# Performance work log

Measured on AMD Instinct MI355X. Metric: run time of the kernel, lower is better.

## Reference

```python
import jax, jax.numpy as jnp
import numpy as np

B, N, C, F, E, K = 4, 4096, 1024, 4096, 8, 2

def setup_inputs() -> dict:
    key = jax.random.key(0)
    ks = jax.random.split(key, 6)
    x = jax.random.normal(ks[0], (B, N, C), dtype=jnp.float32)
    router_w = jax.random.normal(ks[1], (E, C), dtype=jnp.float32) * 0.02  # nn.Linear weight [out,in]
    w1 = jax.random.normal(ks[2], (E, C, F), dtype=jnp.float32) * (1.0 / np.sqrt(C))
    b1 = jnp.zeros((E, F), dtype=jnp.float32)
    w2 = jax.random.normal(ks[3], (E, F, C), dtype=jnp.float32) * (1.0 / np.sqrt(F))
    b2 = jnp.zeros((E, C), dtype=jnp.float32)
    return {"x": x, "router_w": router_w, "w1": w1, "b1": b1, "w2": w2, "b2": b2}

def reference(x, router_w, w1, b1, w2, b2):
    Bx, Nx, Cx = x.shape
    xf = x.reshape(-1, Cx)                                  # [T, C]
    logits = xf @ router_w.T                                # [T, E]
    probs = jax.nn.softmax(logits, axis=-1)
    top_w, top_i = jax.lax.top_k(probs, K)                  # [T, K]
    top_w = top_w / (jnp.sum(top_w, axis=-1, keepdims=True) + 1e-9)
    out = jnp.zeros_like(xf)
    for e in range(E):
        # combine weight for expert e per token (0 if not routed)
        gate = jnp.sum(jnp.where(top_i == e, top_w, 0.0), axis=-1)   # [T]
        h = jax.nn.gelu(xf @ w1[e] + b1[e], approximate=False)       # [T, F]
        y = h @ w2[e] + b2[e]                                        # [T, C]
        out = out + gate[:, None] * y
    return out.reshape(Bx, Nx, Cx)
```

## Files before the change

### kernel.cpp

```cpp
#include <hip/hip_runtime.h>
#include <hip/hip_fp16.h>

#define T_TOK 16384
#define C_DIM 1024
#define F_DIM 4096
#define E_NUM 8

typedef _Float16 half8 __attribute__((ext_vector_type(8)));
typedef _Float16 half4v __attribute__((ext_vector_type(4)));
typedef float f32x4 __attribute__((ext_vector_type(4)));

static constexpr size_t META_OFF  = 0;
static constexpr size_t XB_OFF    = 256;
static constexpr size_t W1T_OFF   = XB_OFF  + (size_t)2*T_TOK*C_DIM;
static constexpr size_t W2T_OFF   = W1T_OFF + (size_t)2*E_NUM*C_DIM*F_DIM;
static constexpr size_t HB_OFF    = W2T_OFF + (size_t)2*E_NUM*C_DIM*F_DIM;
static constexpr size_t YB_OFF    = HB_OFF  + (size_t)2*T_TOK*2*F_DIM;
static constexpr size_t TOK_OFF   = YB_OFF  + (size_t)2*T_TOK*2*C_DIM;
static constexpr size_t GATE_OFF  = TOK_OFF + (size_t)4*E_NUM*T_TOK;
static constexpr size_t TSLOT_OFF = GATE_OFF+ (size_t)4*E_NUM*T_TOK;
static constexpr size_t EPAIR_OFF = TSLOT_OFF + (size_t)4*T_TOK*2;
static constexpr size_t GPAIR_OFF = EPAIR_OFF + (size_t)4*T_TOK;
static constexpr size_t WS_NEED   = GPAIR_OFF + (size_t)8*T_TOK;

__device__ __forceinline__ void async16(void* lds, const void* g) {
  __builtin_amdgcn_global_load_lds((const __attribute__((address_space(1))) unsigned int*)g,
                                   (__attribute__((address_space(3))) unsigned int*)lds,
                                   16, 0, 0);
}

__device__ __forceinline__ void stagger(int bid) {
  int s = (bid >> 8) & 3;
  for (int i = 0; i < s * 5; ++i) __builtin_amdgcn_s_sleep(2);
}

__global__ __launch_bounds__(256) void transpose_cast_kernel(const float* __restrict__ in,
                                                             _Float16* __restrict__ outp,
                                                             int R, int Cc) {
  __shared__ float tile[64][65];
  int e = blockIdx.z;
  const float* ip = in + (size_t)e * R * Cc;
  _Float16* op = outp + (size_t)e * R * Cc;
  int c0 = blockIdx.x * 64, r0 = blockIdx.y * 64;
  int tid = threadIdx.x;
  int lr = tid >> 4, lc = (tid & 15) * 4;
  #pragma unroll
  for (int d = 0; d < 4; ++d) {
    int row = lr + d * 16;
    float4 v = *(const float4*)(ip + (size_t)(r0 + row) * Cc + c0 + lc);
    tile[row][lc]     = v.x;
    tile[row][lc + 1] = v.y;
    tile[row][lc + 2] = v.z;
    tile[row][lc + 3] = v.w;
  }
  __syncthreads();
  int oc = tid >> 3, or8 = (tid & 7) * 8;
  #pragma unroll
  for (int d = 0; d < 2; ++d) {
    int c = oc + d * 32;
    half8 h;
    #pragma unroll
    for (int j = 0; j < 8; ++j) h[j] = (_Float16)tile[or8 + j][c];
    *(half8*)(op + (size_t)(c0 + c) * R + r0 + or8) = h;
  }
}

__global__ __launch_bounds__(256) void router_kernel(const float* __restrict__ x,
                                                     const float* __restrict__ rw,
                                                     int* __restrict__ epair,
                                                     float2* __restrict__ gpair,
                                                     _Float16* __restrict__ xb) {
  int wv = threadIdx.x >> 6, l = threadIdx.x & 63;
  int t = blockIdx.x * 4 + wv;
  const float* xr = x + (size_t)t * C_DIM;
  double acc[E_NUM] = {};
  #pragma unroll
  for (int j = 0; j < 4; ++j) {
    float4 xv = *(const float4*)(xr + j * 256 + l * 4);
    half4v hv;
    hv[0] = (_Float16)xv.x; hv[1] = (_Float16)xv.y;
    hv[2] = (_Float16)xv.z; hv[3] = (_Float16)xv.w;
    *(half4v*)(xb + (size_t)t * C_DIM + j * 256 + l * 4) = hv;
    #pragma unroll
    for (int e = 0; e < E_NUM; ++e) {
      float4 w4 = *(const float4*)(rw + (size_t)e * C_DIM + j * 256 + l * 4);
      acc[e] += (double)xv.x * w4.x + (double)xv.y * w4.y +
                (double)xv.z * w4.z + (double)xv.w * w4.w;
    }
  }
  #pragma unroll
  for (int e = 0; e < E_NUM; ++e)
    #pragma unroll
    for (int off = 32; off; off >>= 1)
      acc[e] += __shfl_xor(acc[e], off, 64);

  if (l == 0) {
    double m = acc[0];
    #pragma unroll
    for (int e = 1; e < E_NUM; ++e) m = acc[e] > m ? acc[e] : m;
    double p[E_NUM], s = 0.0;
    #pragma unroll
    for (int e = 0; e < E_NUM; ++e) { p[e] = exp(acc[e] - m); s += p[e]; }
    int i0 = 0; double b0 = p[0];
    #pragma unroll
    for (int e = 1; e < E_NUM; ++e) if (p[e] > b0) { b0 = p[e]; i0 = e; }
    int i1 = -1; double b1v = -1.0;
    #pragma unroll
    for (int e = 0; e < E_NUM; ++e) if (e != i0 && p[e] > b1v) { b1v = p[e]; i1 = e; }
    double q0 = b0 / s, q1 = b1v / s;
    double den = q0 + q1 + 1e-9;
    epair[t] = i0 | (i1 << 8);
    gpair[t] = make_float2((float)(q0 / den), (float)(q1 / den));
  }
}

__global__ __launch_bounds__(1024) void assign_kernel(const int* __restrict__ epair,
                                                      const float2* __restrict__ gpair,
                                                      int* __restrict__ counts,
                                                      int* __restrict__ tok,
                                                      float* __restrict__ gate,
                                                      int* __restrict__ tslot) {
  __shared__ int wsum[16];
  __shared__ int wbase[16];
  __shared__ int stot;
  int myE = blockIdx.x;
  int tid = threadIdx.x, wid = tid >> 6, lane = tid & 63;
  int base = 0;
  for (int it = 0; it < (T_TOK * 2) / 1024; ++it) {
    int idx = it * 1024 + tid;
    int t = idx >> 1, k = idx & 1;
    int ep = epair[t];
    int e = (k ? (ep >> 8) : ep) & 0xff;
    bool f = (e == myE);
    unsigned long long mask = __ballot(f);
    int lanep = __popcll(mask & ((1ull << lane) - 1ull));
    if (lane == 0) wsum[wid] = __popcll(mask);
    __syncthreads();
    if (tid == 0) {
      int s = 0;
      #pragma unroll
      for (int i = 0; i < 16; ++i) { wbase[i] = s; s += wsum[i]; }
      stot = s;
    }
    __syncthreads();
    if (f) {
      int slot = base + wbase[wid] + lanep;
      float2 g = gpair[t];
      tok[myE * T_TOK + slot] = t;
      gate[myE * T_TOK + slot] = k ? g.y : g.x;
      tslot[idx] = (myE << 24) | slot;
    }
    base += stot;
  }
  if (tid == 0) counts[myE] = base;
}

__global__ void plan_kernel(int* meta) {
  if (threadIdx.x == 0 && blockIdx.x == 0) {
    int ro = 0, t128 = 0;
    meta[8] = 0; meta[17] = 0;
    for (int e = 0; e < E_NUM; ++e) {
      int c = meta[e];
      ro += c; t128 += (c + 127) >> 7;
      meta[9 + e] = ro; meta[18 + e] = t128;
    }
  }
}


__global__ __launch_bounds__(512) void gemm1_kernel(const _Float16* __restrict__ xb,
                                                    const _Float16* __restrict__ w1t,
                                                    const float* __restrict__ b1,
                                                    _Float16* __restrict__ hbuf,
                                                    const int* __restrict__ tok,
                                                    const int* __restrict__ meta) {
  __shared__ _Float16 smem[24576];
  __shared__ int tokLds[128];

  int bid = blockIdx.x;
  int swz = (bid & 7) * 528 + (bid >> 3);
  int band = swz >> 7, rem = swz & 127;
  int nt = rem >> 3;
  int mt = band * 8 + (rem & 7);
  if (mt >= meta[17 + E_NUM]) return;
  stagger(bid);
  int e = 0;
  while (mt >= meta[18 + e]) ++e;
  int ne = meta[e];
  int r0 = (mt - meta[17 + e]) << 7;
  int valid = ne - r0; if (valid > 128) valid = 128;

  int tid = threadIdx.x;
  if (tid < 128) {
    int r = tid < valid ? tid : valid - 1;
    tokLds[tid] = tok[e * T_TOK + r0 + r];
  }
  __syncthreads();

  int srow = tid >> 3, c8 = tid & 7;
  int ch = c8 ^ (srow & 7);
  const _Float16* aLo = xb + (size_t)tokLds[srow] * C_DIM + ch * 8;
  const _Float16* aHi = xb + (size_t)tokLds[srow + 64] * C_DIM + ch * 8;
  const _Float16* bS  = w1t + ((size_t)e * F_DIM + nt * 256 + srow) * C_DIM + ch * 8;

  char* SM = (char*)smem;
  char* dst = SM + (size_t)tid * 16;

  int w = tid >> 6, l = tid & 63;
  int wm = w >> 2, wn = w & 3;
  int rl = l & 15, q = l >> 4;
  int sw0 = (q ^ (rl & 7)) * 16;
  int sw1 = ((4 + q) ^ (rl & 7)) * 16;
  int aBy = wm * 8192 + rl * 128;
  int bBy = 16384 + wn * 8192 + rl * 128;

  f32x4 acc[4][4] = {};
  constexpr int NT = C_DIM / 64;
  for (int kt = 0; kt < NT; ++kt) {
    __syncthreads();
    int ko = kt * 64;
    async16(dst,          aLo + ko);
    async16(dst + 8192,   aHi + ko);
    async16(dst + 16384,  bS + ko);
    async16(dst + 24576,  bS + (size_t) 64 * C_DIM + ko);
    async16(dst + 32768,  bS + (size_t)128 * C_DIM + ko);
    async16(dst + 40960,  bS + (size_t)192 * C_DIM + ko);
    __syncthreads();
    #pragma unroll
    for (int ks = 0; ks < 2; ++ks) {
      int sw = ks ? sw1 : sw0;
      half8 af[4], bf[4];
      #pragma unroll
      for (int m = 0; m < 4; ++m)
        af[m] = *(const half8*)(SM + aBy + m * 2048 + sw);
      #pragma unroll
      for (int n = 0; n < 4; ++n)
        bf[n] = *(const half8*)(SM + bBy + n * 2048 + sw);
      #pragma unroll
      for (int m = 0; m < 4; ++m)
        #pragma unroll
        for (int n = 0; n < 4; ++n)
          acc[m][n] = __builtin_amdgcn_mfma_f32_16x16x32_f16(af[m], bf[n], acc[m][n], 0, 0, 0);
    }
  }

  int hbase = meta[8 + e] + r0;
  float bv[4];
  #pragma unroll
  for (int n = 0; n < 4; ++n)
    bv[n] = b1[(size_t)e * F_DIM + nt * 256 + wn * 64 + n * 16 + rl];
  #pragma unroll
  for (int m = 0; m < 4; ++m) {
    int rb = wm * 64 + m * 16 + q * 4;
    #pragma unroll
    for (int n = 0; n < 4; ++n) {
      int col = nt * 256 + wn * 64 + n * 16 + rl;
      #pragma unroll
      for (int r = 0; r < 4; ++r) {
        int rr = rb + r;
        if (rr < valid) {
          float pre = acc[m][n][r] + bv[n];
          float g = 0.5f * pre * (1.0f + erff(pre * 0.70710678118654752f));
          hbuf[(size_t)(hbase + rr) * F_DIM + col] = (_Float16)g;
        }
      }
    }
  }
}

__global__ __launch_bounds__(512) void gemm2_kernel(const _Float16* __restrict__ hbuf,
                                                    const _Float16* __restrict__ w2t,
                                                    const float* __restrict__ b2,
                                                    _Float16* __restrict__ ybuf,
                                                    const float* __restrict__ gate,
                                                    const int* __restrict__ meta) {
  __shared__ _Float16 smem[24576];
  __shared__ float gateLds[128];

  int bid = blockIdx.x;
  int swz = (bid & 7) * 132 + (bid >> 3);
  int band = swz >> 5, rem = swz & 31;
  int nt = rem >> 3;
  int mt = band * 8 + (rem & 7);
  if (mt >= meta[17 + E_NUM]) return;
  stagger(bid);
  int e = 0;
  while (mt >= meta[18 + e]) ++e;
  int ne = meta[e];
  int r0 = (mt - meta[17 + e]) << 7;
  int valid = ne - r0; if (valid > 128) valid = 128;
  int hbase = meta[8 + e] + r0;

  int tid = threadIdx.x;
  if (tid < 128) {
    int r = tid < valid ? tid : valid - 1;
    gateLds[tid] = gate[e * T_TOK + r0 + r];
  }
  __syncthreads();

  int srow = tid >> 3, c8 = tid & 7;
  int ch = c8 ^ (srow & 7);
  int rcLo = srow      < valid ? srow      : valid - 1;
  int rcHi = srow + 64 < valid ? srow + 64 : valid - 1;
  const _Float16* aLo = hbuf + (size_t)(hbase + rcLo) * F_DIM + ch * 8;
  const _Float16* aHi = hbuf + (size_t)(hbase + rcHi) * F_DIM + ch * 8;
  const _Float16* bS  = w2t + ((size_t)e * C_DIM + nt * 256 + srow) * F_DIM + ch * 8;

  char* SM = (char*)smem;
  char* dst = SM + (size_t)tid * 16;

  int w = tid >> 6, l = tid & 63;
  int wm = w >> 2, wn = w & 3;
  int rl = l & 15, q = l >> 4;
  int sw0 = (q ^ (rl & 7)) * 16;
  int sw1 = ((4 + q) ^ (rl & 7)) * 16;
  int aBy = wm * 8192 + rl * 128;
  int bBy = 16384 + wn * 8192 + rl * 128;

  f32x4 acc[4][4] = {};
  constexpr int NT = F_DIM / 64;
  for (int kt = 0; kt < NT; ++kt) {
    __syncthreads();
    int ko = kt * 64;
    async16(dst,          aLo + ko);
    async16(dst + 8192,   aHi + ko);
    async16(dst + 16384,  bS + ko);
    async16(dst + 24576,  bS + (size_t) 64 * F_DIM + ko);
    async16(dst + 32768,  bS + (size_t)128 * F_DIM + ko);
    async16(dst + 40960,  bS + (size_t)192 * F_DIM + ko);
    __syncthreads();
    #pragma unroll
    for (int ks = 0; ks < 2; ++ks) {
      int sw = ks ? sw1 : sw0;
      half8 af[4], bf[4];
      #pragma unroll
      for (int m = 0; m < 4; ++m)
        af[m] = *(const half8*)(SM + aBy + m * 2048 + sw);
      #pragma unroll
      for (int n = 0; n < 4; ++n)
        bf[n] = *(const half8*)(SM + bBy + n * 2048 + sw);
      #pragma unroll
      for (int m = 0; m < 4; ++m)
        #pragma unroll
        for (int n = 0; n < 4; ++n)
          acc[m][n] = __builtin_amdgcn_mfma_f32_16x16x32_f16(af[m], bf[n], acc[m][n], 0, 0, 0);
    }
  }

  float bv[4];
  #pragma unroll
  for (int n = 0; n < 4; ++n)
    bv[n] = b2[(size_t)e * C_DIM + nt * 256 + wn * 64 + n * 16 + rl];
  #pragma unroll
  for (int m = 0; m < 4; ++m) {
    int rb = wm * 64 + m * 16 + q * 4;
    #pragma unroll
    for (int n = 0; n < 4; ++n) {
      int col = nt * 256 + wn * 64 + n * 16 + rl;
      #pragma unroll
      for (int r = 0; r < 4; ++r) {
        int rr = rb + r;
        if (rr < valid) {
          float val = gateLds[rr] * (acc[m][n][r] + bv[n]);
          ybuf[(size_t)(hbase + rr) * C_DIM + col] = (_Float16)val;
        }
      }
    }
  }
}

__global__ __launch_bounds__(256) void combine_kernel(const _Float16* __restrict__ ybuf,
                                                      const int* __restrict__ tslot,
                                                      const int* __restrict__ meta,
                                                      float* __restrict__ out) {
  int gid = blockIdx.x * 256 + threadIdx.x;
  int t = gid >> 7;
  int cc = (gid & 127) << 3;
  int s0 = tslot[t * 2], s1 = tslot[t * 2 + 1];
  size_t r0 = (size_t)meta[8 + (s0 >> 24)] + (s0 & 0xFFFFFF);
  size_t r1 = (size_t)meta[8 + (s1 >> 24)] + (s1 & 0xFFFFFF);
  half8 y0 = *(const half8*)(ybuf + r0 * C_DIM + cc);
  half8 y1 = *(const half8*)(ybuf + r1 * C_DIM + cc);
  float4 o0, o1;
  o0.x = (float)y0[0] + (float)y1[0];
  o0.y = (float)y0[1] + (float)y1[1];
  o0.z = (float)y0[2] + (float)y1[2];
  o0.w = (float)y0[3] + (float)y1[3];
  o1.x = (float)y0[4] + (float)y1[4];
  o1.y = (float)y0[5] + (float)y1[5];
  o1.z = (float)y0[6] + (float)y1[6];
  o1.w = (float)y0[7] + (float)y1[7];
  *(float4*)(out + (size_t)t * C_DIM + cc) = o0;
  *(float4*)(out + (size_t)t * C_DIM + cc + 4) = o1;
}

extern "C" void kernel_launch(void* const* d_in, const int* in_sizes, int n_in,
                              void* d_out, int out_size, void* d_ws, size_t ws_size,
                              hipStream_t stream) {
  (void)in_sizes; (void)n_in; (void)out_size;
  if (!d_ws || ws_size < WS_NEED) return;

  const float* x  = (const float*)d_in[0];
  const float* rw = (const float*)d_in[1];
  const float* w1 = (const float*)d_in[2];
  const float* b1 = (const float*)d_in[3];
  const float* w2 = (const float*)d_in[4];
  const float* b2 = (const float*)d_in[5];
  float* out = (float*)d_out;

  char* ws = (char*)d_ws;
  int*       meta  = (int*)(ws + META_OFF);
  _Float16*  xb    = (_Float16*)(ws + XB_OFF);
  _Float16*  w1t   = (_Float16*)(ws + W1T_OFF);
  _Float16*  w2t   = (_Float16*)(ws + W2T_OFF);
  _Float16*  hbuf  = (_Float16*)(ws + HB_OFF);
  _Float16*  ybuf  = (_Float16*)(ws + YB_OFF);
  int*       tok   = (int*)(ws + TOK_OFF);
  float*     gate  = (float*)(ws + GATE_OFF);
  int*       tslot = (int*)(ws + TSLOT_OFF);
  int*       epair = (int*)(ws + EPAIR_OFF);
  float2*    gpair = (float2*)(ws + GPAIR_OFF);

  hipMemsetAsync(meta, 0, 256, stream);

  transpose_cast_kernel<<<dim3(F_DIM / 64, C_DIM / 64, E_NUM), 256, 0, stream>>>(w1, w1t, C_DIM, F_DIM);
  transpose_cast_kernel<<<dim3(C_DIM / 64, F_DIM / 64, E_NUM), 256, 0, stream>>>(w2, w2t, F_DIM, C_DIM);
  router_kernel<<<T_TOK / 4, 256, 0, stream>>>(x, rw, epair, gpair, xb);
  assign_kernel<<<E_NUM, 1024, 0, stream>>>(epair, gpair, meta, tok, gate, tslot);
  plan_kernel<<<1, 64, 0, stream>>>(meta);

  gemm1_kernel<<<264 * 16, 512, 0, stream>>>(xb, w1t, b1, hbuf, tok, meta);
  gemm2_kernel<<<264 * 4, 512, 0, stream>>>(hbuf, w2t, b2, ybuf, gate, meta);
  combine_kernel<<<(T_TOK * (C_DIM / 8)) / 256, 256, 0, stream>>>(ybuf, tslot, meta, out);
}
```

Before: 934.4 us.

## Enlarge gemm1 to 256x256 tiles with double-buffered async LDS pipeline

The first expert GEMM moves from 128x256 tiles with a single LDS buffer and two barriers per k-step to 256x256 tiles. Two 64 KB LDS stages are filled by async loads that are interleaved with MFMA phases, using explicit vmcnt waits, s_barrier and s_setprio. The plan kernel now also computes per-expert prefix counts of 256-row tiles, and the grid and its swizzle constants are resized to match. The aim is to hide global-load latency and raise arithmetic intensity. In exchange it uses much more LDS and more accumulator registers (occupancy drops to one block per CU), pads experts to 256 rows, and drops the launch stagger.

```diff
diff --git a/kernel.cpp b/kernel.cpp
--- a/kernel.cpp
+++ b/kernel.cpp
@@ -157,16 +157,50 @@
 
 __global__ void plan_kernel(int* meta) {
   if (threadIdx.x == 0 && blockIdx.x == 0) {
-    int ro = 0, t128 = 0;
-    meta[8] = 0; meta[17] = 0;
+    int ro = 0, t128 = 0, t256 = 0;
+    meta[8] = 0; meta[17] = 0; meta[26] = 0;
     for (int e = 0; e < E_NUM; ++e) {
       int c = meta[e];
-      ro += c; t128 += (c + 127) >> 7;
-      meta[9 + e] = ro; meta[18 + e] = t128;
-    }
-  }
-}
-
+      ro += c; t128 += (c + 127) >> 7; t256 += (c + 255) >> 8;
+      meta[9 + e] = ro; meta[18 + e] = t128; meta[27 + e] = t256;
+    }
+  }
+}
+
+
+#define VM4 asm volatile("s_waitcnt vmcnt(4)" ::: "memory")
+#define VM6 asm volatile("s_waitcnt vmcnt(6)" ::: "memory")
+#define VM8 asm volatile("s_waitcnt vmcnt(8)" ::: "memory")
+
+#define STA(b,s,t) async16(SM + (b)*65536 + (s)*8192 + (size_t)tid*16, aSeg[s] + (t)*64)
+#define STB(b,s,t) async16(SM + (b)*65536 + 32768 + (s)*8192 + (size_t)tid*16, bSeg[s] + (t)*64)
+
+#define PH_LOAD(TB, MH, NH)                                                    \
+    _Pragma("unroll")                                                          \
+    for (int i2 = 0; i2 < 4; ++i2) {                                           \
+      af[i2*2]   = *(const half8*)(SM + (TB) + (MH)*16384 + aOff[i2] + sw0);   \
+      af[i2*2+1] = *(const half8*)(SM + (TB) + (MH)*16384 + aOff[i2] + sw1);   \
+    }                                                                          \
+    _Pragma("unroll")                                                          \
+    for (int j2 = 0; j2 < 2; ++j2) {                                           \
+      bf[j2*2]   = *(const half8*)(SM + (TB) + 32768 + (NH)*16384 + bOff[j2] + sw0); \
+      bf[j2*2+1] = *(const half8*)(SM + (TB) + 32768 + (NH)*16384 + bOff[j2] + sw1); \
+    }
+
+#define PH_MMA(MH, NH)                                                         \
+    __builtin_amdgcn_s_barrier();                                              \
+    __builtin_amdgcn_s_setprio(1);                                             \
+    _Pragma("unroll")                                                          \
+    for (int i2 = 0; i2 < 4; ++i2)                                             \
+      _Pragma("unroll")                                                        \
+      for (int j2 = 0; j2 < 2; ++j2) {                                         \
+        acc[(MH)*4+i2][(NH)*2+j2] = __builtin_amdgcn_mfma_f32_16x16x32_f16(    \
+            af[i2*2], bf[j2*2], acc[(MH)*4+i2][(NH)*2+j2], 0, 0, 0);           \
+        acc[(MH)*4+i2][(NH)*2+j2] = __builtin_amdgcn_mfma_f32_16x16x32_f16(    \
+            af[i2*2+1], bf[j2*2+1], acc[(MH)*4+i2][(NH)*2+j2], 0, 0, 0);       \
+      }                                                                        \
+    __builtin_amdgcn_s_setprio(0);                                             \
+    __builtin_amdgcn_s_barrier();
 
 __global__ __launch_bounds__(512) void gemm1_kernel(const _Float16* __restrict__ xb,
                                                     const _Float16* __restrict__ w1t,
@@ -174,24 +208,23 @@
                                                     _Float16* __restrict__ hbuf,
                                                     const int* __restrict__ tok,
                                                     const int* __restrict__ meta) {
-  __shared__ _Float16 smem[24576];
-  __shared__ int tokLds[128];
+  __shared__ _Float16 smem[65536];
+  __shared__ int tokLds[256];
 
   int bid = blockIdx.x;
-  int swz = (bid & 7) * 528 + (bid >> 3);
+  int swz = (bid & 7) * 272 + (bid >> 3);
   int band = swz >> 7, rem = swz & 127;
   int nt = rem >> 3;
   int mt = band * 8 + (rem & 7);
-  if (mt >= meta[17 + E_NUM]) return;
-  stagger(bid);
+  if (mt >= meta[26 + E_NUM]) return;
   int e = 0;
-  while (mt >= meta[18 + e]) ++e;
+  while (mt >= meta[27 + e]) ++e;
   int ne = meta[e];
-  int r0 = (mt - meta[17 + e]) << 7;
-  int valid = ne - r0; if (valid > 128) valid = 128;
+  int r0 = (mt - meta[26 + e]) << 8;
+  int valid = ne - r0; if (valid > 256) valid = 256;
 
   int tid = threadIdx.x;
-  if (tid < 128) {
+  if (tid < 256) {
     int r = tid < valid ? tid : valid - 1;
     tokLds[tid] = tok[e * T_TOK + r0 + r];
   }
@@ -199,69 +232,91 @@
 
   int srow = tid >> 3, c8 = tid & 7;
   int ch = c8 ^ (srow & 7);
-  const _Float16* aLo = xb + (size_t)tokLds[srow] * C_DIM + ch * 8;
-  const _Float16* aHi = xb + (size_t)tokLds[srow + 64] * C_DIM + ch * 8;
-  const _Float16* bS  = w1t + ((size_t)e * F_DIM + nt * 256 + srow) * C_DIM + ch * 8;
-
+  const _Float16* aSeg[4];
+  const _Float16* bSeg[4];
+  #pragma unroll
+  for (int s = 0; s < 4; ++s) {
+    aSeg[s] = xb + (size_t)tokLds[s * 64 + srow] * C_DIM + ch * 8;
+    bSeg[s] = w1t + ((size_t)e * F_DIM + nt * 256 + s * 64 + srow) * C_DIM + ch * 8;
+  }
   char* SM = (char*)smem;
-  char* dst = SM + (size_t)tid * 16;
 
   int w = tid >> 6, l = tid & 63;
-  int wm = w >> 2, wn = w & 3;
+  int wh = w >> 2, wn = w & 3;
   int rl = l & 15, q = l >> 4;
   int sw0 = (q ^ (rl & 7)) * 16;
   int sw1 = ((4 + q) ^ (rl & 7)) * 16;
-  int aBy = wm * 8192 + rl * 128;
-  int bBy = 16384 + wn * 8192 + rl * 128;
-
-  f32x4 acc[4][4] = {};
-  constexpr int NT = C_DIM / 64;
-  for (int kt = 0; kt < NT; ++kt) {
-    __syncthreads();
-    int ko = kt * 64;
-    async16(dst,          aLo + ko);
-    async16(dst + 8192,   aHi + ko);
-    async16(dst + 16384,  bS + ko);
-    async16(dst + 24576,  bS + (size_t) 64 * C_DIM + ko);
-    async16(dst + 32768,  bS + (size_t)128 * C_DIM + ko);
-    async16(dst + 40960,  bS + (size_t)192 * C_DIM + ko);
-    __syncthreads();
-    #pragma unroll
-    for (int ks = 0; ks < 2; ++ks) {
-      int sw = ks ? sw1 : sw0;
-      half8 af[4], bf[4];
-      #pragma unroll
-      for (int m = 0; m < 4; ++m)
-        af[m] = *(const half8*)(SM + aBy + m * 2048 + sw);
-      #pragma unroll
-      for (int n = 0; n < 4; ++n)
-        bf[n] = *(const half8*)(SM + bBy + n * 2048 + sw);
-      #pragma unroll
-      for (int m = 0; m < 4; ++m)
-        #pragma unroll
-        for (int n = 0; n < 4; ++n)
-          acc[m][n] = __builtin_amdgcn_mfma_f32_16x16x32_f16(af[m], bf[n], acc[m][n], 0, 0, 0);
-    }
+  int aOff[4], bOff[2];
+  #pragma unroll
+  for (int i2 = 0; i2 < 4; ++i2) {
+    int mq = 2 * i2 + wh;
+    aOff[i2] = (mq >> 2) * 8192 + (mq & 3) * 2048 + rl * 128;
+  }
+  #pragma unroll
+  for (int j2 = 0; j2 < 2; ++j2)
+    bOff[j2] = j2 * 8192 + wn * 2048 + rl * 128;
+
+  STA(0,0,0); STA(0,1,0); STA(0,2,0); STA(0,3,0);
+  STB(0,0,0); STB(0,1,0); STB(0,2,0); STB(0,3,0);
+  STA(1,0,1); STA(1,1,1); STB(1,0,1); STB(1,1,1);
+  VM4;
+  __builtin_amdgcn_s_barrier();
+
+  f32x4 acc[8][4] = {};
+  constexpr int NTILE = C_DIM / 64;
+  for (int p = 0; p < NTILE / 2; ++p) {
+    int t1  = 2 * p + 1;
+    int t0n = 2 * p + 2 < NTILE ? 2 * p + 2 : NTILE - 1;
+    int t1n = 2 * p + 3 < NTILE ? 2 * p + 3 : NTILE - 1;
+    half8 af[8], bf[4];
+    PH_LOAD(0, 0, 0);
+    STA(1,2,t1); STA(1,3,t1);
+    VM6;
+    PH_MMA(0, 0);
+    PH_LOAD(0, 0, 1);
+    STB(1,2,t1); STB(1,3,t1);
+    PH_MMA(0, 1);
+    PH_LOAD(0, 1, 0);
+    STA(0,0,t0n); STA(0,1,t0n);
+    PH_MMA(1, 0);
+    PH_LOAD(0, 1, 1);
+    STB(0,0,t0n); STB(0,1,t0n);
+    VM8;
+    PH_MMA(1, 1);
+    PH_LOAD(65536, 0, 0);
+    STA(0,2,t0n); STA(0,3,t0n);
+    VM6;
+    PH_MMA(0, 0);
+    PH_LOAD(65536, 0, 1);
+    STB(0,2,t0n); STB(0,3,t0n);
+    PH_MMA(0, 1);
+    PH_LOAD(65536, 1, 0);
+    STA(1,0,t1n); STA(1,1,t1n);
+    PH_MMA(1, 0);
+    PH_LOAD(65536, 1, 1);
+    STB(1,0,t1n); STB(1,1,t1n);
+    VM8;
+    PH_MMA(1, 1);
   }
 
   int hbase = meta[8 + e] + r0;
   float bv[4];
   #pragma unroll
-  for (int n = 0; n < 4; ++n)
-    bv[n] = b1[(size_t)e * F_DIM + nt * 256 + wn * 64 + n * 16 + rl];
-  #pragma unroll
-  for (int m = 0; m < 4; ++m) {
-    int rb = wm * 64 + m * 16 + q * 4;
-    #pragma unroll
-    for (int n = 0; n < 4; ++n) {
-      int col = nt * 256 + wn * 64 + n * 16 + rl;
+  for (int J = 0; J < 4; ++J)
+    bv[J] = b1[(size_t)e * F_DIM + nt * 256 + (4 * J + wn) * 16 + rl];
+  #pragma unroll
+  for (int I = 0; I < 8; ++I) {
+    int rb = (2 * I + wh) * 16 + q * 4;
+    #pragma unroll
+    for (int J = 0; J < 4; ++J) {
+      int col = nt * 256 + (4 * J + wn) * 16 + rl;
       #pragma unroll
       for (int r = 0; r < 4; ++r) {
-        int rr = rb + r;
-        if (rr < valid) {
-          float pre = acc[m][n][r] + bv[n];
+        int row = rb + r;
+        if (row < valid) {
+          float pre = acc[I][J][r] + bv[J];
           float g = 0.5f * pre * (1.0f + erff(pre * 0.70710678118654752f));
-          hbuf[(size_t)(hbase + rr) * F_DIM + col] = (_Float16)g;
+          hbuf[(size_t)(hbase + row) * F_DIM + col] = (_Float16)g;
         }
       }
     }
@@ -429,7 +484,7 @@
   assign_kernel<<<E_NUM, 1024, 0, stream>>>(epair, gpair, meta, tok, gate, tslot);
   plan_kernel<<<1, 64, 0, stream>>>(meta);
 
-  gemm1_kernel<<<264 * 16, 512, 0, stream>>>(xb, w1t, b1, hbuf, tok, meta);
+  gemm1_kernel<<<136 * 16, 512, 0, stream>>>(xb, w1t, b1, hbuf, tok, meta);
   gemm2_kernel<<<264 * 4, 512, 0, stream>>>(hbuf, w2t, b2, ybuf, gate, meta);
   combine_kernel<<<(T_TOK * (C_DIM / 8)) / 256, 256, 0, stream>>>(ybuf, tslot, meta, out);
 }
```

Measured after the change: 1.146 ms. +22.7%, slower.
